# Optimization experiments

Measured on AMD Instinct MI355X. Metric: run time of the kernel, lower is better.

## Reference

```python
import jax, jax.numpy as jnp
import numpy as np

VNUMS = [4248, 4258, 5327, 3721, 5404, 2818]
B, C, H, W = 12, 64, 192, 192
DV, HID, BOX = 128, 256, 32


def _roi_patches(imgs, pros, imgbatch, box_len=BOX):
    # torchvision roi_align (aligned=False, sampling_ratio -> 1 sample per 1x1 bin):
    # bilinear sample at bin centers x1 + (j+0.5), y1 + (i+0.5)
    ar = jnp.arange(box_len, dtype=pros.dtype) + 0.5
    xs = pros[:, 0:1] - box_len / 2.0 + ar  # [G, box]
    ys = pros[:, 1:2] - box_len / 2.0 + ar  # [G, box]
    img_g = imgs[imgbatch]  # [G, C, H, W]

    def sample_one(img_chw, ys1, xs1):
        yy, xx = jnp.meshgrid(ys1, xs1, indexing="ij")  # [box, box]
        def per_c(ch):
            return jax.scipy.ndimage.map_coordinates(ch, [yy, xx], order=1, mode="nearest")
        return jax.vmap(per_c)(img_chw)  # [C, box, box]

    return jax.vmap(sample_one)(img_g, ys, xs)  # [G, C, box, box]


def setup_inputs() -> dict:
    key = jax.random.key(0)
    ks = jax.random.split(key, 6)
    G = 2 * B
    gtypes = np.array([(g // 2) % 6 if g % 2 == 0 else ((g // 2) + 3) % 6 for g in range(G)], dtype=np.int64)
    vnums_g = np.array([VNUMS[t] for t in gtypes])
    off = np.concatenate([[0], np.cumsum(vnums_g)])
    Nv = int(off[-1])  # 103104
    gar_of_vert = np.repeat(np.arange(G), vnums_g)
    idxs = []
    for t in range(6):
        gl = np.nonzero(gtypes == t)[0]
        idxs.append(np.concatenate([off[g] + np.arange(VNUMS[t]) for g in gl]).astype(np.int32))
    Din = DV + C
    pros = jax.random.uniform(ks[1], (G, 2), jnp.float32) * (H - 2.0 * BOX) + BOX
    inp = {
        "imgs": jax.random.normal(ks[0], (B, C, H, W), jnp.float32),
        "pros": pros,
        "x_verts": jax.random.normal(ks[2], (Nv, DV), jnp.float32),
        "W1": jax.random.normal(ks[3], (6, Din, HID), jnp.float32) / np.sqrt(Din).astype(np.float32),
        "W2": jax.random.normal(ks[4], (6, HID, HID), jnp.float32) / np.sqrt(HID).astype(np.float32),
        "W3": jax.random.normal(ks[5], (6, HID, 3), jnp.float32) / np.sqrt(HID).astype(np.float32),
        "imgbatch": jnp.asarray(np.arange(G) // 2, jnp.int32),
        "gar_of_vert": jnp.asarray(gar_of_vert, jnp.int32),
    }
    for t in range(6):
        inp[f"idx_t{t}"] = jnp.asarray(idxs[t])
    return inp


def reference(imgs, pros, x_verts, W1, W2, W3, imgbatch, gar_of_vert,
              idx_t0, idx_t1, idx_t2, idx_t3, idx_t4, idx_t5):
    # 1) roi_align patch extraction + pooled per-garment image feature
    patches = _roi_patches(imgs, pros, imgbatch)        # [G, C, 32, 32]
    garf = patches.mean(axis=(2, 3))                     # [G, C]
    # 2) per-vertex feature = [vertex feat | garment image feat]
    feat = jnp.concatenate([x_verts, garf[gar_of_vert]], axis=-1)  # [Nv, DV+C]
    # 3) MoE-style dispatch per garment type -> per-type expert MLP -> scatter-combine
    out = jnp.zeros((x_verts.shape[0], 3), feat.dtype)
    for t, idx in enumerate([idx_t0, idx_t1, idx_t2, idx_t3, idx_t4, idx_t5]):
        ft = feat[idx]                                   # gather (dispatch)
        h = jax.nn.relu(ft @ W1[t])
        h = jax.nn.relu(h @ W2[t])
        out = out.at[idx].set(h @ W3[t])                 # scatter (combine)
    return out
```

## Files before the change

### kernel.cpp

```cpp
#include <hip/hip_runtime.h>

typedef __attribute__((ext_vector_type(8))) short short8;
typedef __attribute__((ext_vector_type(4))) float float4_;

__device__ __forceinline__ unsigned short f2bf(float f) {
    unsigned u = __float_as_uint(f);
    u += 0x7FFFu + ((u >> 16) & 1u);
    return (unsigned short)(u >> 16);
}

#define GARF_BLOCKS 1536
#define PREP_BLOCKS 2784

__global__ void prep_garf(const float* __restrict__ imgs,
                          const float* __restrict__ pros,
                          const int* __restrict__ imgbatch,
                          const float* __restrict__ W1,
                          const float* __restrict__ W2,
                          const float* __restrict__ W3,
                          unsigned short* __restrict__ w1t,
                          unsigned short* __restrict__ w2t,
                          unsigned short* __restrict__ w3t,
                          float* __restrict__ garf) {
    const int tid = threadIdx.x;
    if (blockIdx.x < GARF_BLOCKS) {
        __shared__ float part[4];
        int pc = blockIdx.x;
        int g = pc >> 6, c = pc & 63;
        int b = imgbatch[g];
        float cx = pros[g * 2 + 0], cy = pros[g * 2 + 1];
        int i = tid >> 3;
        int j0 = (tid & 7) * 4;
        float y = cy - 16.0f + (float)i + 0.5f;
        float yf = floorf(y);
        float wy1 = y - yf, wy0 = 1.0f - wy1;
        int iy0 = min(max((int)yf, 0), 191), iy1 = min(max((int)yf + 1, 0), 191);
        const float* base = imgs + (size_t)(b * 64 + c) * 36864;
        const float* r0 = base + iy0 * 192;
        const float* r1 = base + iy1 * 192;
        float sum = 0.0f;
#pragma unroll
        for (int jj = 0; jj < 4; ++jj) {
            float x = cx - 16.0f + (float)(j0 + jj) + 0.5f;
            float xf = floorf(x);
            float wx1 = x - xf, wx0 = 1.0f - wx1;
            int ix0 = min(max((int)xf, 0), 191), ix1 = min(max((int)xf + 1, 0), 191);
            sum += wy0 * (wx0 * r0[ix0] + wx1 * r0[ix1]) +
                   wy1 * (wx0 * r1[ix0] + wx1 * r1[ix1]);
        }
        for (int s = 32; s >= 1; s >>= 1) sum += __shfl_xor(sum, s);
        if ((tid & 63) == 0) part[tid >> 6] = sum;
        __syncthreads();
        if (tid == 0)
            garf[g * 64 + c] = (part[0] + part[1] + part[2] + part[3]) * (1.0f / 1024.0f);
    } else {
        int id = (blockIdx.x - GARF_BLOCKS) * 256 + tid;
        if (id < 294912) {
            int t = id / 49152, r = id % 49152;
            int k = r >> 8, n = r & 255;
            w1t[t * 49152 + n * 192 + k] = f2bf(W1[id]);
        } else if (id < 688128) {
            int i2 = id - 294912;
            int t = i2 >> 16, r = i2 & 65535;
            int k = r >> 8, n = r & 255;
            w2t[t * 65536 + n * 256 + k] = f2bf(W2[i2]);
        } else if (id < 712704) {
            int i3 = id - 688128;
            int t = i3 >> 12, r = i3 & 4095;
            int n = r >> 8, k = r & 255;
            w3t[i3] = (n < 3) ? f2bf(W3[t * 768 + k * 3 + n]) : (unsigned short)0;
        }
    }
}

struct MoEArgs {
    const float* x_verts;
    const int* gar;
    const int* idx[6];
    const unsigned short* w1t;
    const unsigned short* w2t;
    const unsigned short* w3t;
    const float* garf;
    float* out;
    int cnt[6];
    int tile_end[6];
};

__global__ __launch_bounds__(256, 4) void moe_kernel(MoEArgs a) {
    __shared__ __align__(16) char smem[32768 + 512];
    char* sF = smem;
    int* sidx = (int*)(smem + 32768);
    int* sg = sidx + 64;

    const int tid = threadIdx.x;
    int bt = blockIdx.x;
    int t = 0;
    while (t < 5 && bt >= a.tile_end[t]) ++t;
    const int tile = bt - (t ? a.tile_end[t - 1] : 0);
    const int cnt = a.cnt[t];
    const int i0 = tile * 64;
    const int* idx = a.idx[t];

    if (tid < 64) {
        int m = i0 + tid;
        if (m > cnt - 1) m = cnt - 1;
        int vid = idx[m];
        sidx[tid] = vid;
        sg[tid] = a.gar[vid];
    }
    __syncthreads();

    for (int e = tid; e < 1536; e += 256) {
        int m = e / 24, u = e % 24;
        const float* src;
        if (u < 16) src = a.x_verts + (size_t)sidx[m] * 128 + u * 8;
        else        src = a.garf + sg[m] * 64 + (u - 16) * 8;
        float4 v0 = ((const float4*)src)[0];
        float4 v1 = ((const float4*)src)[1];
        short8 pk;
        pk[0] = f2bf(v0.x); pk[1] = f2bf(v0.y); pk[2] = f2bf(v0.z); pk[3] = f2bf(v0.w);
        pk[4] = f2bf(v1.x); pk[5] = f2bf(v1.y); pk[6] = f2bf(v1.z); pk[7] = f2bf(v1.w);
        *(short8*)(sF + m * 384 + ((u ^ (m & 7)) * 16)) = pk;
    }
    __syncthreads();

    const int lane = tid & 63, w = tid >> 6, q = lane >> 4, l = lane & 15;

    float4_ acc[4][4] = {};
    const unsigned short* w1 = a.w1t + (size_t)t * 49152;
    for (int ks = 0; ks < 6; ++ks) {
        short8 af[4], bfr[4];
        for (int mt = 0; mt < 4; ++mt) {
            int hid = w * 64 + mt * 16 + l;
            af[mt] = *(const short8*)(w1 + hid * 192 + ks * 32 + q * 8);
        }
        for (int nt = 0; nt < 4; ++nt) {
            int v = nt * 16 + l;
            bfr[nt] = *(const short8*)(sF + v * 384 + (((ks * 4 + q) ^ (v & 7)) * 16));
        }
        for (int mt = 0; mt < 4; ++mt)
            for (int nt = 0; nt < 4; ++nt)
                acc[mt][nt] = __builtin_amdgcn_mfma_f32_16x16x32_bf16(
                    af[mt], bfr[nt], acc[mt][nt], 0, 0, 0);
    }
    __syncthreads();

    for (int mt = 0; mt < 4; ++mt)
        for (int nt = 0; nt < 4; ++nt) {
            int v = nt * 16 + l;
            int hu8 = w * 16 + mt * 4 + q;
            int ku16 = hu8 >> 1, par = hu8 & 1;
            uint2 pk;
            pk.x = (unsigned)f2bf(fmaxf(acc[mt][nt][0], 0.0f)) |
                   ((unsigned)f2bf(fmaxf(acc[mt][nt][1], 0.0f)) << 16);
            pk.y = (unsigned)f2bf(fmaxf(acc[mt][nt][2], 0.0f)) |
                   ((unsigned)f2bf(fmaxf(acc[mt][nt][3], 0.0f)) << 16);
            *(uint2*)(sF + v * 512 + ((ku16 ^ (v & 7)) * 16) + par * 8) = pk;
        }
    __syncthreads();

    float4_ acc2[4][4] = {};
    const unsigned short* w2 = a.w2t + (size_t)t * 65536;
    for (int ks = 0; ks < 8; ++ks) {
        short8 af[4], bfr[4];
        for (int mt = 0; mt < 4; ++mt) {
            int hid = w * 64 + mt * 16 + l;
            af[mt] = *(const short8*)(w2 + hid * 256 + ks * 32 + q * 8);
        }
        for (int nt = 0; nt < 4; ++nt) {
            int v = nt * 16 + l;
            bfr[nt] = *(const short8*)(sF + v * 512 + (((ks * 4 + q) ^ (v & 7)) * 16));
        }
        for (int mt = 0; mt < 4; ++mt)
            for (int nt = 0; nt < 4; ++nt)
                acc2[mt][nt] = __builtin_amdgcn_mfma_f32_16x16x32_bf16(
                    af[mt], bfr[nt], acc2[mt][nt], 0, 0, 0);
    }
    __syncthreads();

    for (int mt = 0; mt < 4; ++mt)
        for (int nt = 0; nt < 4; ++nt) {
            int v = nt * 16 + l;
            int hu8 = w * 16 + mt * 4 + q;
            int ku16 = hu8 >> 1, par = hu8 & 1;
            uint2 pk;
            pk.x = (unsigned)f2bf(fmaxf(acc2[mt][nt][0], 0.0f)) |
                   ((unsigned)f2bf(fmaxf(acc2[mt][nt][1], 0.0f)) << 16);
            pk.y = (unsigned)f2bf(fmaxf(acc2[mt][nt][2], 0.0f)) |
                   ((unsigned)f2bf(fmaxf(acc2[mt][nt][3], 0.0f)) << 16);
            *(uint2*)(sF + v * 512 + ((ku16 ^ (v & 7)) * 16) + par * 8) = pk;
        }
    __syncthreads();

    float4_ acc3 = {};
    const unsigned short* w3 = a.w3t + (size_t)t * 4096;
    int v3 = w * 16 + l;
    for (int ks = 0; ks < 8; ++ks) {
        short8 a3 = *(const short8*)(w3 + l * 256 + ks * 32 + q * 8);
        short8 b3 = *(const short8*)(sF + v3 * 512 + (((ks * 4 + q) ^ (v3 & 7)) * 16));
        acc3 = __builtin_amdgcn_mfma_f32_16x16x32_bf16(a3, b3, acc3, 0, 0, 0);
    }
    if (q == 0) {
        int m = i0 + v3;
        if (m < cnt) {
            float* o = a.out + (size_t)sidx[v3] * 3;
            o[0] = acc3[0]; o[1] = acc3[1]; o[2] = acc3[2];
        }
    }
}

extern "C" void kernel_launch(void* const* d_in, const int* in_sizes, int n_in,
                              void* d_out, int out_size, void* d_ws, size_t ws_size,
                              hipStream_t stream) {
    const float* imgs    = (const float*)d_in[0];
    const float* pros    = (const float*)d_in[1];
    const float* x_verts = (const float*)d_in[2];
    const float* W1      = (const float*)d_in[3];
    const float* W2      = (const float*)d_in[4];
    const float* W3      = (const float*)d_in[5];
    const int* imgbatch  = (const int*)d_in[6];
    const int* gar       = (const int*)d_in[7];

    unsigned short* w1t = (unsigned short*)d_ws;
    unsigned short* w2t = (unsigned short*)((char*)d_ws + 589824);
    unsigned short* w3t = (unsigned short*)((char*)d_ws + 1376256);
    float* garf         = (float*)((char*)d_ws + 1425408);

    prep_garf<<<GARF_BLOCKS + PREP_BLOCKS, 256, 0, stream>>>(
        imgs, pros, imgbatch, W1, W2, W3, w1t, w2t, w3t, garf);

    MoEArgs a;
    a.x_verts = x_verts;
    a.gar = gar;
    for (int t = 0; t < 6; ++t) a.idx[t] = (const int*)d_in[8 + t];
    a.w1t = w1t; a.w2t = w2t; a.w3t = w3t;
    a.garf = garf;
    a.out = (float*)d_out;
    int tiles = 0;
    for (int t = 0; t < 6; ++t) {
        a.cnt[t] = in_sizes[8 + t];
        tiles += (a.cnt[t] + 63) / 64;
        a.tile_end[t] = tiles;
    }
    moe_kernel<<<tiles, 256, 0, stream>>>(a);
}
```

Before: 268.6 us.

## Pair two tiles per block with staggered stage schedule to overlap phases

Each 512-thread block now handles two 64-vertex tiles, one per 256-thread half, each with its own shared buffer. The halves run one phase apart (stage, layer1, epilogue, layer2, epilogue, layer3), so one half's gather or epilogue can overlap the other's MFMA work. The per-block sidx/sg index buffers are dropped in favour of reading idx and gar directly inside the stage loop. This adds extra block-wide barriers and idle half-phases at the start and end. It also doubles shared memory per block, and launch bounds of 512x4 may limit registers per thread and cause spills.

```diff
diff --git a/kernel.cpp b/kernel.cpp
--- a/kernel.cpp
+++ b/kernel.cpp
@@ -86,127 +86,143 @@
     int tile_end[6];
 };
 
-__global__ __launch_bounds__(256, 4) void moe_kernel(MoEArgs a) {
-    __shared__ __align__(16) char smem[32768 + 512];
-    char* sF = smem;
-    int* sidx = (int*)(smem + 32768);
-    int* sg = sidx + 64;
+__global__ __launch_bounds__(512, 4) void moe_kernel(MoEArgs a) {
+    __shared__ __align__(16) char smem[2][32768];
 
     const int tid = threadIdx.x;
-    int bt = blockIdx.x;
+    const int half = tid >> 8;
+    const int ltid = tid & 255;
+    char* sF = smem[half];
+
+    const int total = a.tile_end[5];
+    const int bt = blockIdx.x * 2 + half;
+    const bool active = bt < total;
+
     int t = 0;
-    while (t < 5 && bt >= a.tile_end[t]) ++t;
-    const int tile = bt - (t ? a.tile_end[t - 1] : 0);
+    if (active) { while (t < 5 && bt >= a.tile_end[t]) ++t; }
+    const int tile = active ? (bt - (t ? a.tile_end[t - 1] : 0)) : 0;
     const int cnt = a.cnt[t];
     const int i0 = tile * 64;
     const int* idx = a.idx[t];
 
-    if (tid < 64) {
-        int m = i0 + tid;
-        if (m > cnt - 1) m = cnt - 1;
-        int vid = idx[m];
-        sidx[tid] = vid;
-        sg[tid] = a.gar[vid];
-    }
-    __syncthreads();
-
-    for (int e = tid; e < 1536; e += 256) {
-        int m = e / 24, u = e % 24;
-        const float* src;
-        if (u < 16) src = a.x_verts + (size_t)sidx[m] * 128 + u * 8;
-        else        src = a.garf + sg[m] * 64 + (u - 16) * 8;
-        float4 v0 = ((const float4*)src)[0];
-        float4 v1 = ((const float4*)src)[1];
-        short8 pk;
-        pk[0] = f2bf(v0.x); pk[1] = f2bf(v0.y); pk[2] = f2bf(v0.z); pk[3] = f2bf(v0.w);
-        pk[4] = f2bf(v1.x); pk[5] = f2bf(v1.y); pk[6] = f2bf(v1.z); pk[7] = f2bf(v1.w);
-        *(short8*)(sF + m * 384 + ((u ^ (m & 7)) * 16)) = pk;
-    }
-    __syncthreads();
-
-    const int lane = tid & 63, w = tid >> 6, q = lane >> 4, l = lane & 15;
-
-    float4_ acc[4][4] = {};
+    const int lane = ltid & 63, w = ltid >> 6, q = lane >> 4, l = lane & 15;
     const unsigned short* w1 = a.w1t + (size_t)t * 49152;
-    for (int ks = 0; ks < 6; ++ks) {
-        short8 af[4], bfr[4];
-        for (int mt = 0; mt < 4; ++mt) {
-            int hid = w * 64 + mt * 16 + l;
-            af[mt] = *(const short8*)(w1 + hid * 192 + ks * 32 + q * 8);
-        }
-        for (int nt = 0; nt < 4; ++nt) {
-            int v = nt * 16 + l;
-            bfr[nt] = *(const short8*)(sF + v * 384 + (((ks * 4 + q) ^ (v & 7)) * 16));
-        }
+    const unsigned short* w2 = a.w2t + (size_t)t * 65536;
+    const unsigned short* w3 = a.w3t + (size_t)t * 4096;
+
+    float4_ acc[4][4];
+
+    auto STAGE = [&]() {
+#pragma unroll
+        for (int e0 = 0; e0 < 1536; e0 += 256) {
+            int e = e0 + ltid;
+            int m = e / 24, u = e - m * 24;
+            int mi = i0 + m; mi = (mi < cnt) ? mi : (cnt - 1);
+            int vid = idx[mi];
+            const float* src = (u < 16)
+                ? a.x_verts + (size_t)vid * 128 + u * 8
+                : a.garf + (size_t)a.gar[vid] * 64 + (u - 16) * 8;
+            float4 v0 = ((const float4*)src)[0];
+            float4 v1 = ((const float4*)src)[1];
+            short8 pk;
+            pk[0] = f2bf(v0.x); pk[1] = f2bf(v0.y); pk[2] = f2bf(v0.z); pk[3] = f2bf(v0.w);
+            pk[4] = f2bf(v1.x); pk[5] = f2bf(v1.y); pk[6] = f2bf(v1.z); pk[7] = f2bf(v1.w);
+            *(short8*)(sF + m * 384 + ((u ^ (m & 7)) * 16)) = pk;
+        }
+    };
+
+    auto C1 = [&]() {
+#pragma unroll
         for (int mt = 0; mt < 4; ++mt)
-            for (int nt = 0; nt < 4; ++nt)
-                acc[mt][nt] = __builtin_amdgcn_mfma_f32_16x16x32_bf16(
-                    af[mt], bfr[nt], acc[mt][nt], 0, 0, 0);
-    }
-    __syncthreads();
-
-    for (int mt = 0; mt < 4; ++mt)
-        for (int nt = 0; nt < 4; ++nt) {
-            int v = nt * 16 + l;
-            int hu8 = w * 16 + mt * 4 + q;
-            int ku16 = hu8 >> 1, par = hu8 & 1;
-            uint2 pk;
-            pk.x = (unsigned)f2bf(fmaxf(acc[mt][nt][0], 0.0f)) |
-                   ((unsigned)f2bf(fmaxf(acc[mt][nt][1], 0.0f)) << 16);
-            pk.y = (unsigned)f2bf(fmaxf(acc[mt][nt][2], 0.0f)) |
-                   ((unsigned)f2bf(fmaxf(acc[mt][nt][3], 0.0f)) << 16);
-            *(uint2*)(sF + v * 512 + ((ku16 ^ (v & 7)) * 16) + par * 8) = pk;
-        }
-    __syncthreads();
-
-    float4_ acc2[4][4] = {};
-    const unsigned short* w2 = a.w2t + (size_t)t * 65536;
-    for (int ks = 0; ks < 8; ++ks) {
-        short8 af[4], bfr[4];
-        for (int mt = 0; mt < 4; ++mt) {
-            int hid = w * 64 + mt * 16 + l;
-            af[mt] = *(const short8*)(w2 + hid * 256 + ks * 32 + q * 8);
-        }
-        for (int nt = 0; nt < 4; ++nt) {
-            int v = nt * 16 + l;
-            bfr[nt] = *(const short8*)(sF + v * 512 + (((ks * 4 + q) ^ (v & 7)) * 16));
-        }
+#pragma unroll
+            for (int nt = 0; nt < 4; ++nt) acc[mt][nt] = (float4_){0.f, 0.f, 0.f, 0.f};
+        for (int ks = 0; ks < 6; ++ks) {
+            short8 af[4], bfr[4];
+#pragma unroll
+            for (int mt = 0; mt < 4; ++mt)
+                af[mt] = *(const short8*)(w1 + (w * 64 + mt * 16 + l) * 192 + ks * 32 + q * 8);
+#pragma unroll
+            for (int nt = 0; nt < 4; ++nt) {
+                int v = nt * 16 + l;
+                bfr[nt] = *(const short8*)(sF + v * 384 + (((ks * 4 + q) ^ (v & 7)) * 16));
+            }
+#pragma unroll
+            for (int mt = 0; mt < 4; ++mt)
+#pragma unroll
+                for (int nt = 0; nt < 4; ++nt)
+                    acc[mt][nt] = __builtin_amdgcn_mfma_f32_16x16x32_bf16(
+                        af[mt], bfr[nt], acc[mt][nt], 0, 0, 0);
+        }
+    };
+
+    auto EPI = [&]() {
+#pragma unroll
         for (int mt = 0; mt < 4; ++mt)
-            for (int nt = 0; nt < 4; ++nt)
-                acc2[mt][nt] = __builtin_amdgcn_mfma_f32_16x16x32_bf16(
-                    af[mt], bfr[nt], acc2[mt][nt], 0, 0, 0);
-    }
-    __syncthreads();
-
-    for (int mt = 0; mt < 4; ++mt)
-        for (int nt = 0; nt < 4; ++nt) {
-            int v = nt * 16 + l;
-            int hu8 = w * 16 + mt * 4 + q;
-            int ku16 = hu8 >> 1, par = hu8 & 1;
-            uint2 pk;
-            pk.x = (unsigned)f2bf(fmaxf(acc2[mt][nt][0], 0.0f)) |
-                   ((unsigned)f2bf(fmaxf(acc2[mt][nt][1], 0.0f)) << 16);
-            pk.y = (unsigned)f2bf(fmaxf(acc2[mt][nt][2], 0.0f)) |
-                   ((unsigned)f2bf(fmaxf(acc2[mt][nt][3], 0.0f)) << 16);
-            *(uint2*)(sF + v * 512 + ((ku16 ^ (v & 7)) * 16) + par * 8) = pk;
-        }
-    __syncthreads();
-
-    float4_ acc3 = {};
-    const unsigned short* w3 = a.w3t + (size_t)t * 4096;
-    int v3 = w * 16 + l;
-    for (int ks = 0; ks < 8; ++ks) {
-        short8 a3 = *(const short8*)(w3 + l * 256 + ks * 32 + q * 8);
-        short8 b3 = *(const short8*)(sF + v3 * 512 + (((ks * 4 + q) ^ (v3 & 7)) * 16));
-        acc3 = __builtin_amdgcn_mfma_f32_16x16x32_bf16(a3, b3, acc3, 0, 0, 0);
-    }
-    if (q == 0) {
-        int m = i0 + v3;
-        if (m < cnt) {
-            float* o = a.out + (size_t)sidx[v3] * 3;
+#pragma unroll
+            for (int nt = 0; nt < 4; ++nt) {
+                int v = nt * 16 + l;
+                int hu8 = w * 16 + mt * 4 + q;
+                int ku16 = hu8 >> 1, par = hu8 & 1;
+                uint2 pk;
+                pk.x = (unsigned)f2bf(fmaxf(acc[mt][nt][0], 0.0f)) |
+                       ((unsigned)f2bf(fmaxf(acc[mt][nt][1], 0.0f)) << 16);
+                pk.y = (unsigned)f2bf(fmaxf(acc[mt][nt][2], 0.0f)) |
+                       ((unsigned)f2bf(fmaxf(acc[mt][nt][3], 0.0f)) << 16);
+                *(uint2*)(sF + v * 512 + ((ku16 ^ (v & 7)) * 16) + par * 8) = pk;
+            }
+    };
+
+    auto C2 = [&]() {
+#pragma unroll
+        for (int mt = 0; mt < 4; ++mt)
+#pragma unroll
+            for (int nt = 0; nt < 4; ++nt) acc[mt][nt] = (float4_){0.f, 0.f, 0.f, 0.f};
+        for (int ks = 0; ks < 8; ++ks) {
+            short8 af[4], bfr[4];
+#pragma unroll
+            for (int mt = 0; mt < 4; ++mt)
+                af[mt] = *(const short8*)(w2 + (w * 64 + mt * 16 + l) * 256 + ks * 32 + q * 8);
+#pragma unroll
+            for (int nt = 0; nt < 4; ++nt) {
+                int v = nt * 16 + l;
+                bfr[nt] = *(const short8*)(sF + v * 512 + (((ks * 4 + q) ^ (v & 7)) * 16));
+            }
+#pragma unroll
+            for (int mt = 0; mt < 4; ++mt)
+#pragma unroll
+                for (int nt = 0; nt < 4; ++nt)
+                    acc[mt][nt] = __builtin_amdgcn_mfma_f32_16x16x32_bf16(
+                        af[mt], bfr[nt], acc[mt][nt], 0, 0, 0);
+        }
+    };
+
+    auto C3 = [&]() {
+        float4_ acc3 = (float4_){0.f, 0.f, 0.f, 0.f};
+        int v3 = w * 16 + l;
+        for (int ks = 0; ks < 8; ++ks) {
+            short8 a3 = *(const short8*)(w3 + l * 256 + ks * 32 + q * 8);
+            short8 b3 = *(const short8*)(sF + v3 * 512 + (((ks * 4 + q) ^ (v3 & 7)) * 16));
+            acc3 = __builtin_amdgcn_mfma_f32_16x16x32_bf16(a3, b3, acc3, 0, 0, 0);
+        }
+        if (q == 0 && i0 + v3 < cnt) {
+            float* o = a.out + (size_t)idx[i0 + v3] * 3;
             o[0] = acc3[0]; o[1] = acc3[1]; o[2] = acc3[2];
         }
-    }
+    };
+
+    if (half == 0) { if (active) STAGE(); }
+    __syncthreads();
+    if (half == 0) { if (active) C1(); } else { if (active) STAGE(); }
+    __syncthreads();
+    if (half == 0) { if (active) EPI(); } else { if (active) C1(); }
+    __syncthreads();
+    if (half == 0) { if (active) C2(); } else { if (active) EPI(); }
+    __syncthreads();
+    if (half == 0) { if (active) EPI(); } else { if (active) C2(); }
+    __syncthreads();
+    if (half == 0) { if (active) C3(); } else { if (active) EPI(); }
+    __syncthreads();
+    if (half == 1 && active) C3();
 }
 
 extern "C" void kernel_launch(void* const* d_in, const int* in_sizes, int n_in,
@@ -242,5 +258,5 @@
         tiles += (a.cnt[t] + 63) / 64;
         a.tile_end[t] = tiles;
     }
-    moe_kernel<<<tiles, 256, 0, stream>>>(a);
-}
+    moe_kernel<<<(tiles + 1) / 2, 512, 0, stream>>>(a);
+}
```

Result: slower. 275.4 us (+2.5%).
